# Kernel tuning notes

Measured on AMD Instinct MI355X. Metric: run time of the kernel, lower is better.

The kernel has to match this reference:

```python
import jax, jax.numpy as jnp
import numpy as np

C = 4          # number of classes (cloud-organization dataset has 4)
EMPTY = 1.0    # IoU value when a class is absent from both pred and label


def setup_inputs() -> dict:
    key = jax.random.key(0)
    k1, k2 = jax.random.split(key)
    shape = (16, 1024, 1024)
    # preds are hard class predictions (stored as float, integer-valued)
    preds = jax.random.randint(k1, shape, 0, C).astype(jnp.float32)
    labels = jax.random.randint(k2, shape, 0, C).astype(jnp.int32)
    return {"preds": preds, "labels": labels}


def reference(preds, labels):
    # Vectorized form of the per-class loop:
    #   intersection_i = ((label == i) & (pred == i)).sum()
    #   union_i        = ((label == i) | (pred == i)).sum()   (ignore=None)
    cls = jnp.arange(C)                      # [C]
    pm = preds[..., None] == cls             # [B,H,W,C] bool
    lm = labels[..., None] == cls            # [B,H,W,C] bool
    inter = jnp.sum(pm & lm, axis=(0, 1, 2)).astype(jnp.float32)  # [C]
    union = jnp.sum(pm | lm, axis=(0, 1, 2)).astype(jnp.float32)  # [C]
    ious = jnp.where(union == 0, EMPTY, inter / jnp.where(union == 0, 1.0, union))
    ious_pct = 100.0 * ious                  # matches 100 * np.array(ious)
    return 1.0 - ious_pct                    # forward returns 1 - iou, shape [C]
```

## Files before the change

### kernel.cpp

```cpp
#include <hip/hip_runtime.h>


#define NCLS 4
#define NCNT (3 * NCLS)

typedef float        vf4 __attribute__((ext_vector_type(4)));
typedef int          vi4 __attribute__((ext_vector_type(4)));
typedef unsigned int vu4 __attribute__((ext_vector_type(4)));

__global__ __launch_bounds__(256) void iou_count_kernel(
    const vf4* __restrict__ preds,
    const vi4* __restrict__ labels,
    unsigned int* __restrict__ partials,
    int n4)
{
    unsigned int acc_i = 0, acc_p = 0, acc_l = 0;

    const int tid    = blockIdx.x * blockDim.x + threadIdx.x;
    const int stride = gridDim.x * blockDim.x;

    auto proc = [&](float pf, int lv) {
        const int      ip = (int)pf;
        const unsigned tp = 1u << (ip << 3);
        const unsigned tl = 1u << (lv << 3);
        acc_p += tp;
        acc_l += tl;
        acc_i += (ip == lv) ? tl : 0u;
    };
    auto acc4 = [&](const vf4 p, const vi4 l) {
        proc(p.x, l.x); proc(p.y, l.y); proc(p.z, l.z); proc(p.w, l.w);
    };

    int idx = tid;
    for (; idx + 3 * stride < n4; idx += 4 * stride) {
        const vf4 p0 = __builtin_nontemporal_load(&preds[idx]);
        const vf4 p1 = __builtin_nontemporal_load(&preds[idx + stride]);
        const vf4 p2 = __builtin_nontemporal_load(&preds[idx + 2 * stride]);
        const vf4 p3 = __builtin_nontemporal_load(&preds[idx + 3 * stride]);
        const vi4 l0 = __builtin_nontemporal_load(&labels[idx]);
        const vi4 l1 = __builtin_nontemporal_load(&labels[idx + stride]);
        const vi4 l2 = __builtin_nontemporal_load(&labels[idx + 2 * stride]);
        const vi4 l3 = __builtin_nontemporal_load(&labels[idx + 3 * stride]);
        acc4(p0, l0); acc4(p1, l1); acc4(p2, l2); acc4(p3, l3);
    }
    for (; idx < n4; idx += stride)
        acc4(__builtin_nontemporal_load(&preds[idx]),
             __builtin_nontemporal_load(&labels[idx]));

    unsigned pk[6];
    pk[0] = acc_i & 0x00FF00FFu; pk[1] = (acc_i >> 8) & 0x00FF00FFu;
    pk[2] = acc_p & 0x00FF00FFu; pk[3] = (acc_p >> 8) & 0x00FF00FFu;
    pk[4] = acc_l & 0x00FF00FFu; pk[5] = (acc_l >> 8) & 0x00FF00FFu;

#pragma unroll
    for (int k = 0; k < 6; ++k) {
#pragma unroll
        for (int off = 32; off > 0; off >>= 1)
            pk[k] += __shfl_down(pk[k], off);
    }

    __shared__ unsigned int s[4][6];
    const int wave = threadIdx.x >> 6;
    if ((threadIdx.x & 63) == 0) {
#pragma unroll
        for (int k = 0; k < 6; ++k) s[wave][k] = pk[k];
    }
    __syncthreads();

    if (threadIdx.x < 6) {
        const int k = threadIdx.x;
        const unsigned tot = s[0][k] + s[1][k] + s[2][k] + s[3][k];
        const int g = k >> 1, r = k & 1;
        __builtin_nontemporal_store(
            tot & 0xFFFFu,
            &partials[(g * NCLS + r)     * gridDim.x + blockIdx.x]);
        __builtin_nontemporal_store(
            tot >> 16,
            &partials[(g * NCLS + r + 2) * gridDim.x + blockIdx.x]);
    }
}

__global__ __launch_bounds__(768) void iou_reduce_kernel(
    const unsigned int* __restrict__ partials,
    float* __restrict__ out,
    int nblk)
{
    __shared__ unsigned int tot[NCNT];
    const int w    = threadIdx.x >> 6;
    const int lane = threadIdx.x & 63;

    if (w < NCNT) {
        const unsigned int* row = partials + (size_t)w * nblk;
        const vu4* row4 = (const vu4*)row;
        const int n4r = nblk >> 2;

        unsigned s0 = 0, s1 = 0, s2 = 0, s3 = 0;
#pragma unroll 8
        for (int k = lane; k < n4r; k += 64) {
            const vu4 v = __builtin_nontemporal_load(&row4[k]);
            s0 += v.x; s1 += v.y; s2 += v.z; s3 += v.w;
        }
        unsigned sum = (s0 + s1) + (s2 + s3);
        for (int k = (n4r << 2) + lane; k < nblk; k += 64)
            sum += row[k];

#pragma unroll
        for (int off = 32; off > 0; off >>= 1)
            sum += __shfl_down(sum, off);
        if (lane == 0) tot[w] = sum;
    }
    __syncthreads();

    if (threadIdx.x < NCLS) {
        const int c = threadIdx.x;
        const float inter = (float)tot[c];
        const float uni   = (float)tot[NCLS + c] + (float)tot[2 * NCLS + c]
                            - (float)tot[c];
        const float iou   = (uni == 0.0f) ? 1.0f : (inter / uni);
        out[c] = 1.0f - 100.0f * iou;
    }
}

extern "C" void kernel_launch(void* const* d_in, const int* in_sizes, int n_in,
                              void* d_out, int out_size, void* d_ws, size_t ws_size,
                              hipStream_t stream) {
    const vf4* preds  = (const vf4*)d_in[0];
    const vi4* labels = (const vi4*)d_in[1];
    unsigned int* partials = (unsigned int*)d_ws;
    float* out = (float*)d_out;

    const int n  = in_sizes[0];
    const int n4 = n / 4;

    int nblk = 2048;
    const int cap = (int)(ws_size / (NCNT * sizeof(unsigned int)));
    if (cap < nblk) nblk = cap & ~3;
    if (nblk < 1) nblk = 1;

    iou_count_kernel<<<nblk, 256, 0, stream>>>(preds, labels, partials, n4);
    iou_reduce_kernel<<<1, 768, 0, stream>>>(partials, out, nblk);
}
```

Measured before the change: 147.4 us.

## Give each block a contiguous chunk with XCD-aware block remapping

Replaces the grid-stride traversal with contiguous per-block chunks. Block IDs are remapped so that blocks landing on the same XCD (assuming round-robin dispatch across 8 XCDs) cover adjacent chunks. The aim is better DRAM page and L2 locality per XCD for this streaming reduction. It relies on that assumed dispatch order, and a chunk size that is not a multiple of 1024 leaves a scalar tail loop in each block.

```diff
diff --git a/kernel.cpp b/kernel.cpp
--- a/kernel.cpp
+++ b/kernel.cpp
@@ -3,6 +3,7 @@
 
 #define NCLS 4
 #define NCNT (3 * NCLS)
+#define NXCD 8
 
 typedef float        vf4 __attribute__((ext_vector_type(4)));
 typedef int          vi4 __attribute__((ext_vector_type(4)));
@@ -12,12 +13,20 @@
     const vf4* __restrict__ preds,
     const vi4* __restrict__ labels,
     unsigned int* __restrict__ partials,
-    int n4)
+    int n4,
+    int chunk)
 {
     unsigned int acc_i = 0, acc_p = 0, acc_l = 0;
 
-    const int tid    = blockIdx.x * blockDim.x + threadIdx.x;
-    const int stride = gridDim.x * blockDim.x;
+    const int nblk  = gridDim.x;
+    const int xcd   = blockIdx.x & (NXCD - 1);
+    const int slot  = blockIdx.x >> 3;
+    const int vblk  = xcd * (nblk >> 3) + slot;
+
+    const int t     = threadIdx.x;
+    const int begin = vblk * chunk;
+    int end = begin + chunk;
+    if (end > n4) end = n4;
 
     auto proc = [&](float pf, int lv) {
         const int      ip = (int)pf;
@@ -31,19 +40,19 @@
         proc(p.x, l.x); proc(p.y, l.y); proc(p.z, l.z); proc(p.w, l.w);
     };
 
-    int idx = tid;
-    for (; idx + 3 * stride < n4; idx += 4 * stride) {
+    int idx = begin + t;
+    for (; idx + 768 < end; idx += 1024) {
         const vf4 p0 = __builtin_nontemporal_load(&preds[idx]);
-        const vf4 p1 = __builtin_nontemporal_load(&preds[idx + stride]);
-        const vf4 p2 = __builtin_nontemporal_load(&preds[idx + 2 * stride]);
-        const vf4 p3 = __builtin_nontemporal_load(&preds[idx + 3 * stride]);
+        const vf4 p1 = __builtin_nontemporal_load(&preds[idx + 256]);
+        const vf4 p2 = __builtin_nontemporal_load(&preds[idx + 512]);
+        const vf4 p3 = __builtin_nontemporal_load(&preds[idx + 768]);
         const vi4 l0 = __builtin_nontemporal_load(&labels[idx]);
-        const vi4 l1 = __builtin_nontemporal_load(&labels[idx + stride]);
-        const vi4 l2 = __builtin_nontemporal_load(&labels[idx + 2 * stride]);
-        const vi4 l3 = __builtin_nontemporal_load(&labels[idx + 3 * stride]);
+        const vi4 l1 = __builtin_nontemporal_load(&labels[idx + 256]);
+        const vi4 l2 = __builtin_nontemporal_load(&labels[idx + 512]);
+        const vi4 l3 = __builtin_nontemporal_load(&labels[idx + 768]);
         acc4(p0, l0); acc4(p1, l1); acc4(p2, l2); acc4(p3, l3);
     }
-    for (; idx < n4; idx += stride)
+    for (; idx < end; idx += 256)
         acc4(__builtin_nontemporal_load(&preds[idx]),
              __builtin_nontemporal_load(&labels[idx]));
 
@@ -134,9 +143,11 @@
 
     int nblk = 2048;
     const int cap = (int)(ws_size / (NCNT * sizeof(unsigned int)));
-    if (cap < nblk) nblk = cap & ~3;
-    if (nblk < 1) nblk = 1;
+    if (cap < nblk) nblk = cap & ~7;
+    if (nblk < 8) nblk = 8;
 
-    iou_count_kernel<<<nblk, 256, 0, stream>>>(preds, labels, partials, n4);
+    const int chunk = (n4 + nblk - 1) / nblk;
+
+    iou_count_kernel<<<nblk, 256, 0, stream>>>(preds, labels, partials, n4, chunk);
     iou_reduce_kernel<<<1, 768, 0, stream>>>(partials, out, nblk);
 }
```

Result: no change. 148.0 us (+0.4%).
